# Kernel tuning notes

Hardware: AMD Instinct MI355X
Metric: run time of the kernel (lower is better)

Reference implementation:

```python
import jax, jax.numpy as jnp
import numpy as np

N_NODES = 50000
N_EDGES = 400000
N_GRAPHS = 256
D = 200
N_STEPS = 6


def setup_inputs() -> dict:
    key = jax.random.key(0)
    ks = jax.random.split(key, 10)
    s = 1.0 / np.sqrt(D)
    x = jax.random.normal(ks[0], (N_NODES, D), dtype=jnp.float32)
    edge_index = jax.random.randint(ks[1], (2, N_EDGES), 0, N_NODES, dtype=jnp.int64)
    batch = jnp.sort(jax.random.randint(ks[2], (N_NODES,), 0, N_GRAPHS, dtype=jnp.int64))
    ggnn_weight = jax.random.uniform(ks[3], (N_STEPS, D, D), jnp.float32, -s, s)
    w_ih = jax.random.uniform(ks[4], (3 * D, D), jnp.float32, -s, s)
    w_hh = jax.random.uniform(ks[5], (3 * D, D), jnp.float32, -s, s)
    b_ih = jax.random.uniform(ks[6], (3 * D,), jnp.float32, -s, s)
    b_hh = jax.random.uniform(ks[7], (3 * D,), jnp.float32, -s, s)
    cls_w = jax.random.uniform(ks[8], (2, D), jnp.float32, -s, s)
    cls_b = jax.random.uniform(ks[9], (2,), jnp.float32, -s, s)
    return {"x": x, "edge_index": edge_index, "batch": batch,
            "ggnn_weight": ggnn_weight, "w_ih": w_ih, "w_hh": w_hh,
            "b_ih": b_ih, "b_hh": b_hh, "cls_w": cls_w, "cls_b": cls_b}


def _gru_cell(m, h, w_ih, w_hh, b_ih, b_hh):
    gi = m @ w_ih.T + b_ih            # [N, 3D]
    gh = h @ w_hh.T + b_hh            # [N, 3D]
    i_r, i_z, i_n = jnp.split(gi, 3, axis=-1)
    h_r, h_z, h_n = jnp.split(gh, 3, axis=-1)
    r = jax.nn.sigmoid(i_r + h_r)
    z = jax.nn.sigmoid(i_z + h_z)
    n = jnp.tanh(i_n + r * h_n)
    return (1.0 - z) * n + z * h


def reference(x, edge_index, batch, ggnn_weight, w_ih, w_hh, b_ih, b_hh, cls_w, cls_b):
    src, dst = edge_index[0], edge_index[1]

    def step(h, W):
        m = h @ W                                        # [N, D]
        agg = jax.ops.segment_sum(m[src], dst, num_segments=N_NODES)  # scatter-add
        return _gru_cell(agg, h, w_ih, w_hh, b_ih, b_hh), None

    h, _ = jax.lax.scan(step, x, ggnn_weight)
    h = jax.nn.relu(h)
    pooled = jax.ops.segment_max(h, batch, num_segments=N_GRAPHS)    # [G, D]
    logits = pooled @ cls_w.T + cls_b                                # [G, 2]
    return jax.nn.sigmoid(logits)
```

## Files before the change

### kernel.cpp

```cpp
#include <hip/hip_runtime.h>
#include <cstdint>
#include <cstddef>

#define NN 50000
#define NE 400000
#define NG 256
#define DIM 200
#define NSTEPS 6

typedef unsigned int uint;
typedef unsigned short ushort;
typedef __attribute__((ext_vector_type(8))) short short8;
typedef __attribute__((ext_vector_type(4))) float f32x4;

#define GLL16(gsrc, ldst)                                                        \
  __builtin_amdgcn_global_load_lds(                                              \
      (const __attribute__((address_space(1))) void*)(gsrc),                     \
      (__attribute__((address_space(3))) void*)(ldst), 16, 0, 0)

__device__ __forceinline__ float bfu(ushort u) { return __uint_as_float((uint)u << 16); }
__device__ __forceinline__ uint packf(float v) {
  uint u = __float_as_uint(v);
  uint t = u + 0x7fffu + ((u >> 16) & 1u);
  uint hb = t & 0xffff0000u;
  float lo = v - __uint_as_float(hb);
  uint ul = __float_as_uint(lo);
  uint t2 = ul + 0x7fffu + ((ul >> 16) & 1u);
  return hb | (t2 >> 16);
}
__device__ __forceinline__ ushort bf16rn(float v) {
  uint u = __float_as_uint(v);
  return (ushort)((u + 0x7fffu + ((u >> 16) & 1u)) >> 16);
}
__device__ __forceinline__ float fsig(float x) {
  return __builtin_amdgcn_rcpf(1.f + __expf(-x));
}
__device__ __forceinline__ float ftanh(float x) {
  return 1.f - 2.f * __builtin_amdgcn_rcpf(__expf(2.f * x) + 1.f);
}

__global__ void k_zero_i32(int* __restrict__ p, int n) {
  for (int i = blockIdx.x * blockDim.x + threadIdx.x; i < n; i += gridDim.x * blockDim.x)
    p[i] = 0;
}
__global__ void k_zero_f32(float* __restrict__ p, int n) {
  for (int i = blockIdx.x * blockDim.x + threadIdx.x; i < n; i += gridDim.x * blockDim.x)
    p[i] = 0.f;
}
__global__ void k_hist(const int* __restrict__ dst, int* __restrict__ cnt, int nE) {
  int e = blockIdx.x * blockDim.x + threadIdx.x;
  if (e < nE) atomicAdd(&cnt[dst[e]], 1);
}

__global__ __launch_bounds__(256) void k_scan_blk(const int* __restrict__ cnt,
                                                  int* __restrict__ incl,
                                                  int* __restrict__ bsum, int n) {
  __shared__ int buf[256];
  int i = blockIdx.x * 256 + threadIdx.x;
  int v = (i < n) ? cnt[i] : 0;
  buf[threadIdx.x] = v;
  __syncthreads();
#pragma unroll
  for (int d = 1; d < 256; d <<= 1) {
    int t = (threadIdx.x >= d) ? buf[threadIdx.x - d] : 0;
    __syncthreads();
    buf[threadIdx.x] += t;
    __syncthreads();
  }
  if (i < n) incl[i] = buf[threadIdx.x];
  if (threadIdx.x == 255) bsum[blockIdx.x] = buf[255];
}
__global__ __launch_bounds__(256) void k_scan_top(int* __restrict__ bsum, int nb) {
  __shared__ int buf[256];
  int v = (threadIdx.x < nb) ? bsum[threadIdx.x] : 0;
  buf[threadIdx.x] = v;
  __syncthreads();
#pragma unroll
  for (int d = 1; d < 256; d <<= 1) {
    int t = (threadIdx.x >= d) ? buf[threadIdx.x - d] : 0;
    __syncthreads();
    buf[threadIdx.x] += t;
    __syncthreads();
  }
  if (threadIdx.x < nb) bsum[threadIdx.x] = buf[threadIdx.x] - v;
}
__global__ __launch_bounds__(256) void k_scan_fin(const int* __restrict__ cnt,
                                                  const int* __restrict__ incl,
                                                  const int* __restrict__ bsum,
                                                  int* __restrict__ off,
                                                  int* __restrict__ cursor, int n) {
  int i = blockIdx.x * 256 + threadIdx.x;
  if (i < n) {
    int o = incl[i] + bsum[blockIdx.x];
    off[i + 1] = o;
    cursor[i] = o - cnt[i];
  }
  if (i == 0) off[0] = 0;
}

__global__ void k_scatter(const int* __restrict__ dst, const int* __restrict__ src,
                          int* __restrict__ cursor, int* __restrict__ slist, int nE) {
  int e = blockIdx.x * blockDim.x + threadIdx.x;
  if (e < nE) {
    int d = dst[e];
    int pos = atomicAdd(&cursor[d], 1);
    slist[pos] = src[e];
  }
}

__global__ void k_pack_split(const float* __restrict__ x, ushort* __restrict__ hHi,
                             ushort* __restrict__ hLo, int n8) {
  for (int i = blockIdx.x * blockDim.x + threadIdx.x; i < n8;
       i += gridDim.x * blockDim.x) {
    const float* s = x + (size_t)i * 8;
    uint hi[4], lo[4];
#pragma unroll
    for (int j = 0; j < 4; ++j) {
      uint w0 = packf(s[j * 2]), w1 = packf(s[j * 2 + 1]);
      hi[j] = (w0 >> 16) | (w1 & 0xffff0000u);
      lo[j] = (w0 & 0xffffu) | (w1 << 16);
    }
    *reinterpret_cast<uint4*>(hHi + (size_t)i * 8) = make_uint4(hi[0], hi[1], hi[2], hi[3]);
    *reinterpret_cast<uint4*>(hLo + (size_t)i * 8) = make_uint4(lo[0], lo[1], lo[2], lo[3]);
  }
}

__global__ void k_pack_bf(const float* __restrict__ in, ushort* __restrict__ out, int n) {
  for (int i = blockIdx.x * blockDim.x + threadIdx.x; i < n; i += gridDim.x * blockDim.x)
    out[i] = bf16rn(in[i]);
}

#define GBM 64
#define GBN 64
#define GBK 8
__global__ __launch_bounds__(256) void k_gemm_wc(const float* __restrict__ gg,
                                                 const float* __restrict__ w_ih,
                                                 ushort* __restrict__ wcB) {
  __shared__ __align__(16) float As[GBK][GBM];
  __shared__ __align__(16) float Bs[GBK][GBN];
  int s = blockIdx.z;
  const float* A = gg + (size_t)s * DIM * DIM;
  ushort* out = wcB + (size_t)s * 3 * DIM * DIM;
  int tid = threadIdx.x;
  int row0 = blockIdx.y * GBM;
  int col0 = blockIdx.x * GBN;
  int ty = tid >> 4, tx = tid & 15;
  float acc[4][4] = {};
  for (int k0 = 0; k0 < DIM; k0 += GBK) {
    {
      int r = tid >> 2;
      int kk = (tid & 3) * 2;
      int gr = row0 + r;
      float2 v = make_float2(0.f, 0.f);
      if (gr < DIM) v = *reinterpret_cast<const float2*>(&A[(size_t)gr * DIM + k0 + kk]);
      As[kk][r] = v.x; As[kk + 1][r] = v.y;
    }
    {
      int n = tid >> 2;
      int kk = (tid & 3) * 2;
      int gn = col0 + n;
      float2 v = *reinterpret_cast<const float2*>(&w_ih[(size_t)gn * DIM + k0 + kk]);
      Bs[kk][n] = v.x; Bs[kk + 1][n] = v.y;
    }
    __syncthreads();
#pragma unroll
    for (int k = 0; k < GBK; ++k) {
      float4 av = *reinterpret_cast<const float4*>(&As[k][ty * 4]);
      float4 bv = *reinterpret_cast<const float4*>(&Bs[k][tx * 4]);
      float a[4] = {av.x, av.y, av.z, av.w};
      float b[4] = {bv.x, bv.y, bv.z, bv.w};
#pragma unroll
      for (int i = 0; i < 4; ++i)
#pragma unroll
        for (int j = 0; j < 4; ++j) acc[i][j] += a[i] * b[j];
    }
    __syncthreads();
  }
#pragma unroll
  for (int i = 0; i < 4; ++i) {
    int r = row0 + ty * 4 + i;
    if (r >= DIM) continue;
#pragma unroll
    for (int j = 0; j < 4; ++j) {
      int c = col0 + tx * 4 + j;
      out[(size_t)c * DIM + r] = bf16rn(acc[i][j]);
    }
  }
}

__global__ __launch_bounds__(256) void k_aggregate_hi(const ushort* __restrict__ hHi,
                                                      const int* __restrict__ off,
                                                      const int* __restrict__ slist,
                                                      ushort* __restrict__ aggHi) {
  int wid = blockIdx.x * 4 + (threadIdx.x >> 6);
  int half = (threadIdx.x >> 5) & 1;
  int node = wid * 2 + half;
  int lane32 = threadIdx.x & 31;
  bool nok = node < NN;
  bool act = (lane32 < 25) && nok;
  const uint4* hb = reinterpret_cast<const uint4*>(hHi);
  float a[8] = {};
  int beg = 0, end = 0;
  if (nok) { beg = off[node]; end = off[node + 1]; }
  int p = beg;
#define ACC8(q)                                                   \
  {                                                               \
    a[0] += __uint_as_float((q).x << 16);                         \
    a[1] += __uint_as_float((q).x & 0xffff0000u);                 \
    a[2] += __uint_as_float((q).y << 16);                         \
    a[3] += __uint_as_float((q).y & 0xffff0000u);                 \
    a[4] += __uint_as_float((q).z << 16);                         \
    a[5] += __uint_as_float((q).z & 0xffff0000u);                 \
    a[6] += __uint_as_float((q).w << 16);                         \
    a[7] += __uint_as_float((q).w & 0xffff0000u);                 \
  }
  for (; p + 3 < end; p += 4) {
    int s0 = slist[p], s1 = slist[p + 1], s2 = slist[p + 2], s3 = slist[p + 3];
    if (act) {
      uint4 q0 = hb[(size_t)s0 * 25 + lane32];
      uint4 q1 = hb[(size_t)s1 * 25 + lane32];
      uint4 q2 = hb[(size_t)s2 * 25 + lane32];
      uint4 q3 = hb[(size_t)s3 * 25 + lane32];
      ACC8(q0) ACC8(q1) ACC8(q2) ACC8(q3)
    }
  }
  for (; p < end; ++p) {
    int s = slist[p];
    if (act) {
      uint4 q = hb[(size_t)s * 25 + lane32];
      ACC8(q)
    }
  }
#undef ACC8
  if (act) {
    uint w[4];
#pragma unroll
    for (int j = 0; j < 4; ++j)
      w[j] = (uint)bf16rn(a[j * 2]) | ((uint)bf16rn(a[j * 2 + 1]) << 16);
    reinterpret_cast<uint4*>(aggHi)[(size_t)node * 25 + lane32] =
        make_uint4(w[0], w[1], w[2], w[3]);
  }
}

#define NPAN 391
#define PPC 6
#define NCHK 66
#define NCOLB 7
#define GRIDF 462

#define MFMA16(a, b, c) __builtin_amdgcn_mfma_f32_16x16x32_bf16(a, b, c, 0, 0, 0)

__global__ __launch_bounds__(256, 2) void k_fused_mfma(
    const ushort* __restrict__ aggHi, const ushort* __restrict__ hHi,
    const ushort* __restrict__ hLo,
    const ushort* __restrict__ wcB, const ushort* __restrict__ whB,
    const float* __restrict__ b_ih, const float* __restrict__ b_hh,
    ushort* __restrict__ hnHi, ushort* __restrict__ hnLo) {
  __shared__ uint4 Bb[6][25][32];

  int tid = threadIdx.x;
  int lane = tid & 63;
  int wv = tid >> 6;
  int lr = lane & 15;
  int kc = lane >> 4;

  int x = blockIdx.x & 7, ii = blockIdx.x >> 3;
  int work = (x < 6 ? x * 58 : 348 + (x - 6) * 57) + ii;
  int chunk = work / NCOLB;
  int col = work - chunk * NCOLB;
  int cc0 = col * 32;

  {
    uint4* BbF = &Bb[0][0][0];
    for (int i2 = 0; i2 < 19; ++i2) {
      int u = tid + i2 * 256;
      if (u < 4800) {
        int mat = u / 800;
        int rem = u - mat * 800;
        int ch = rem >> 5;
        int c = rem & 31;
        int gc = cc0 + c; if (gc > 199) gc = 199;
        const ushort* wsrc = (mat & 1) ? whB : wcB;
        GLL16(wsrc + (size_t)((mat >> 1) * DIM + gc) * DIM + ch * 8, BbF + u);
      }
    }
  }
  __syncthreads();

  for (int j = 0; j < PPC; ++j) {
    int p = chunk * PPC + j;
    if (p >= NPAN) break;
    int prow0 = p * 128;
    int r0 = prow0 + wv * 32 + lr;
    int r1 = r0 + 16;
    int rc0 = r0 < NN ? r0 : NN - 1;
    int rc1 = r1 < NN ? r1 : NN - 1;
    const ushort* a0 = aggHi + (size_t)rc0 * DIM;
    const ushort* a1 = aggHi + (size_t)rc1 * DIM;
    const ushort* h0 = hHi + (size_t)rc0 * DIM;
    const ushort* h1 = hHi + (size_t)rc1 * DIM;

    f32x4 acc[3][2][2][2] = {};
    short8 aq[3][2][2];

#define LDA(d, t)                                                              \
  {                                                                            \
    const bool v_ = ((t) < 6) || (kc == 0);                                    \
    const int of_ = v_ ? ((t) * 32 + kc * 8) : 0;                              \
    const short8 z_ = {0, 0, 0, 0, 0, 0, 0, 0};                                \
    aq[d][0][0] = v_ ? *reinterpret_cast<const short8*>(a0 + of_) : z_;        \
    aq[d][0][1] = v_ ? *reinterpret_cast<const short8*>(a1 + of_) : z_;        \
    aq[d][1][0] = v_ ? *reinterpret_cast<const short8*>(h0 + of_) : z_;        \
    aq[d][1][1] = v_ ? *reinterpret_cast<const short8*>(h1 + of_) : z_;        \
  }

    LDA(0, 0)
    LDA(1, 1)
#pragma unroll
    for (int t = 0; t < 7; ++t) {
      const int cur = t % 3;
      if (t < 5) LDA((t + 2) % 3, t + 2)
      int bch = t * 4 + kc; if (bch > 24) bch = 24;
#pragma unroll
      for (int g = 0; g < 3; ++g) {
#pragma unroll
        for (int ct = 0; ct < 2; ++ct) {
          short8 b1 = *reinterpret_cast<const short8*>(&Bb[g * 2 + 0][bch][ct * 16 + lr]);
          short8 b2 = *reinterpret_cast<const short8*>(&Bb[g * 2 + 1][bch][ct * 16 + lr]);
#pragma unroll
          for (int rf = 0; rf < 2; ++rf) {
            acc[g][0][rf][ct] = MFMA16(aq[cur][0][rf], b1, acc[g][0][rf][ct]);
            acc[g][1][rf][ct] = MFMA16(aq[cur][1][rf], b2, acc[g][1][rf][ct]);
          }
        }
      }
    }
#undef LDA

#pragma unroll
    for (int ct = 0; ct < 2; ++ct) {
      int c = cc0 + ct * 16 + lr;
      if (c >= DIM) continue;
      float bir = b_ih[c], biz = b_ih[DIM + c], bin = b_ih[2 * DIM + c];
      float bhr = b_hh[c], bhz = b_hh[DIM + c], bhn = b_hh[2 * DIM + c];
#pragma unroll
      for (int rf = 0; rf < 2; ++rf) {
#pragma unroll
        for (int qq = 0; qq < 4; ++qq) {
          int r_ = prow0 + wv * 32 + rf * 16 + kc * 4 + qq;
          if (r_ >= NN) continue;
          size_t base = (size_t)r_ * DIM + c;
          float gir = acc[0][0][rf][ct][qq] + bir;
          float giz = acc[1][0][rf][ct][qq] + biz;
          float gin = acc[2][0][rf][ct][qq] + bin;
          float ghr = acc[0][1][rf][ct][qq] + bhr;
          float ghz = acc[1][1][rf][ct][qq] + bhz;
          float ghn = acc[2][1][rf][ct][qq] + bhn;
          float rr = fsig(gir + ghr);
          float zz = fsig(giz + ghz);
          float nn = ftanh(gin + rr * ghn);
          float hv = bfu(hHi[base]) + bfu(hLo[base]);
          uint w = packf((1.f - zz) * nn + zz * hv);
          hnHi[base] = (ushort)(w >> 16);
          hnLo[base] = (ushort)(w & 0xffffu);
        }
      }
    }
  }
}

__global__ __launch_bounds__(256) void k_pool(const ushort* __restrict__ hHi,
                                              const ushort* __restrict__ hLo,
                                              const int* __restrict__ batch,
                                              float* __restrict__ pooled) {
  int i = blockIdx.x;
  int j = threadIdx.x;
  if (j < DIM) {
    int g = batch[i];
    size_t base = (size_t)i * DIM + j;
    float v = bfu(hHi[base]) + bfu(hLo[base]);
    v = v > 0.f ? v : 0.f;
    atomicMax((int*)&pooled[(size_t)g * DIM + j], __float_as_int(v));
  }
}

__global__ __launch_bounds__(256) void k_classify(const float* __restrict__ pooled,
                                                  const float* __restrict__ w,
                                                  const float* __restrict__ b,
                                                  float* __restrict__ out) {
  __shared__ float r0[256], r1[256];
  int g = blockIdx.x;
  int j = threadIdx.x;
  float p = (j < DIM) ? pooled[(size_t)g * DIM + j] : 0.f;
  r0[j] = (j < DIM) ? p * w[j] : 0.f;
  r1[j] = (j < DIM) ? p * w[DIM + j] : 0.f;
  __syncthreads();
  for (int d = 128; d > 0; d >>= 1) {
    if (j < d) { r0[j] += r0[j + d]; r1[j] += r1[j + d]; }
    __syncthreads();
  }
  if (j == 0) {
    out[g * 2 + 0] = 1.f / (1.f + expf(-(r0[0] + b[0])));
    out[g * 2 + 1] = 1.f / (1.f + expf(-(r1[0] + b[1])));
  }
}

extern "C" void kernel_launch(void* const* d_in, const int* in_sizes, int n_in,
                              void* d_out, int out_size, void* d_ws, size_t ws_size,
                              hipStream_t stream) {
  const float* x = (const float*)d_in[0];
  const int* edge_index = (const int*)d_in[1];
  const int* batch = (const int*)d_in[2];
  const float* ggnn_w = (const float*)d_in[3];
  const float* w_ih = (const float*)d_in[4];
  const float* w_hh = (const float*)d_in[5];
  const float* b_ih = (const float*)d_in[6];
  const float* b_hh = (const float*)d_in[7];
  const float* cls_w = (const float*)d_in[8];
  const float* cls_b = (const float*)d_in[9];
  float* out = (float*)d_out;

  const int* src = edge_index;
  const int* dst = edge_index + NE;

  char* wsb = (char*)d_ws;
  size_t off = 0;
  auto alloc = [&](size_t bytes) -> void* {
    void* p = wsb + off;
    off += (bytes + 255) & ~(size_t)255;
    return p;
  };
  ushort* hHiA = (ushort*)alloc((size_t)NN * DIM * 2);
  ushort* hLoA = (ushort*)alloc((size_t)NN * DIM * 2);
  ushort* hHiB = (ushort*)alloc((size_t)NN * DIM * 2);
  ushort* hLoB = (ushort*)alloc((size_t)NN * DIM * 2);
  ushort* aggHi = (ushort*)alloc((size_t)NN * DIM * 2);
  ushort* wcB = (ushort*)alloc((size_t)NSTEPS * 3 * DIM * DIM * 2);
  ushort* whB = (ushort*)alloc((size_t)3 * DIM * DIM * 2);
  float* pooled = (float*)alloc((size_t)NG * DIM * 4);
  int* indeg = (int*)alloc((size_t)NN * 4);
  int* offs = (int*)alloc((size_t)(NN + 1) * 4);
  int* incl = (int*)alloc((size_t)NN * 4);
  int* bsum = (int*)alloc((size_t)256 * 4);
  int* cursor = (int*)alloc((size_t)NN * 4);
  int* slist = (int*)alloc((size_t)NE * 4);
  if (off > ws_size) return;

  const int NB = (NN + 255) / 256;

  k_pack_split<<<2048, 256, 0, stream>>>(x, hHiA, hLoA, NN * DIM / 8);

  k_zero_i32<<<196, 256, 0, stream>>>(indeg, NN);
  k_hist<<<(NE + 255) / 256, 256, 0, stream>>>(dst, indeg, NE);
  k_scan_blk<<<NB, 256, 0, stream>>>(indeg, incl, bsum, NN);
  k_scan_top<<<1, 256, 0, stream>>>(bsum, NB);
  k_scan_fin<<<NB, 256, 0, stream>>>(indeg, incl, bsum, offs, cursor, NN);
  k_scatter<<<(NE + 255) / 256, 256, 0, stream>>>(dst, src, cursor, slist, NE);

  {
    dim3 g((3 * DIM + GBN - 1) / GBN, (DIM + GBM - 1) / GBM, NSTEPS);
    k_gemm_wc<<<g, 256, 0, stream>>>(ggnn_w, w_ih, wcB);
    k_pack_bf<<<512, 256, 0, stream>>>(w_hh, whB, 3 * DIM * DIM);
  }

  ushort* hHic = hHiA;
  ushort* hLoc = hLoA;
  ushort* hHin = hHiB;
  ushort* hLon = hLoB;
  for (int s = 0; s < NSTEPS; ++s) {
    k_aggregate_hi<<<(NN / 2 + 3) / 4, 256, 0, stream>>>(hHic, offs, slist, aggHi);
    k_fused_mfma<<<GRIDF, 256, 0, stream>>>(aggHi, hHic, hLoc,
                                            wcB + (size_t)s * 3 * DIM * DIM,
                                            whB, b_ih, b_hh, hHin, hLon);
    ushort* t;
    t = hHic; hHic = hHin; hHin = t;
    t = hLoc; hLoc = hLon; hLon = t;
  }

  k_zero_f32<<<200, 256, 0, stream>>>(pooled, NG * DIM);
  k_pool<<<NN, 256, 0, stream>>>(hHic, hLoc, batch, pooled);
  k_classify<<<NG, 256, 0, stream>>>(pooled, cls_w, cls_b, out);
}
```

Baseline: 700.0 us.

## Deepen A prefetch, preload epilogue h values, halve panels per block

The fused GRU MFMA kernel now gives each block 3 row panels instead of 6, which roughly doubles the grid, and the work mapping across the 8 XCD slices is rebalanced to match. The A-operand prefetch ring grows from 3 to 4 stages. The hHi/hLo values the epilogue needs are loaded into registers during the last MFMA iterations, so their latency overlaps compute instead of stalling the epilogue. The low-half bf16 pack now truncates instead of rounding, trimming epilogue ALU work at a tiny precision cost. In exchange, register pressure rises and each block reloads the weight tile into LDS over fewer panels.

```diff
diff --git a/kernel.cpp b/kernel.cpp
--- a/kernel.cpp
+++ b/kernel.cpp
@@ -27,6 +27,13 @@
   uint ul = __float_as_uint(lo);
   uint t2 = ul + 0x7fffu + ((ul >> 16) & 1u);
   return hb | (t2 >> 16);
+}
+__device__ __forceinline__ uint packf_tr(float v) {
+  uint u = __float_as_uint(v);
+  uint t = u + 0x7fffu + ((u >> 16) & 1u);
+  uint hb = t & 0xffff0000u;
+  float lo = v - __uint_as_float(hb);
+  return hb | (__float_as_uint(lo) >> 16);
 }
 __device__ __forceinline__ ushort bf16rn(float v) {
   uint u = __float_as_uint(v);
@@ -243,10 +250,10 @@
 }
 
 #define NPAN 391
-#define PPC 6
-#define NCHK 66
+#define PPC 3
+#define NCHK 131
 #define NCOLB 7
-#define GRIDF 462
+#define GRIDF 917
 
 #define MFMA16(a, b, c) __builtin_amdgcn_mfma_f32_16x16x32_bf16(a, b, c, 0, 0, 0)
 
@@ -265,7 +272,7 @@
   int kc = lane >> 4;
 
   int x = blockIdx.x & 7, ii = blockIdx.x >> 3;
-  int work = (x < 6 ? x * 58 : 348 + (x - 6) * 57) + ii;
+  int work = (x < 5 ? x * 115 : 575 + (x - 5) * 114) + ii;
   int chunk = work / NCOLB;
   int col = work - chunk * NCOLB;
   int cc0 = col * 32;
@@ -301,7 +308,8 @@
     const ushort* h1 = hHi + (size_t)rc1 * DIM;
 
     f32x4 acc[3][2][2][2] = {};
-    short8 aq[3][2][2];
+    short8 aq[4][2][2];
+    ushort hvh[2][2][4], hvl[2][2][4];
 
 #define LDA(d, t)                                                              \
   {                                                                            \
@@ -316,10 +324,28 @@
 
     LDA(0, 0)
     LDA(1, 1)
+    LDA(2, 2)
 #pragma unroll
     for (int t = 0; t < 7; ++t) {
-      const int cur = t % 3;
-      if (t < 5) LDA((t + 2) % 3, t + 2)
+      const int cur = t & 3;
+      if (t < 4) LDA((t + 3) & 3, t + 3)
+      if (t == 5) {
+#pragma unroll
+        for (int ct = 0; ct < 2; ++ct) {
+          int c = cc0 + ct * 16 + lr; if (c > 199) c = 199;
+#pragma unroll
+          for (int rf = 0; rf < 2; ++rf) {
+#pragma unroll
+            for (int qq = 0; qq < 4; ++qq) {
+              int r_ = prow0 + wv * 32 + rf * 16 + kc * 4 + qq;
+              int rc = r_ < NN ? r_ : NN - 1;
+              size_t base = (size_t)rc * DIM + c;
+              hvh[ct][rf][qq] = hHi[base];
+              hvl[ct][rf][qq] = hLo[base];
+            }
+          }
+        }
+      }
       int bch = t * 4 + kc; if (bch > 24) bch = 24;
 #pragma unroll
       for (int g = 0; g < 3; ++g) {
@@ -359,8 +385,8 @@
           float rr = fsig(gir + ghr);
           float zz = fsig(giz + ghz);
           float nn = ftanh(gin + rr * ghn);
-          float hv = bfu(hHi[base]) + bfu(hLo[base]);
-          uint w = packf((1.f - zz) * nn + zz * hv);
+          float hv = bfu(hvh[ct][rf][qq]) + bfu(hvl[ct][rf][qq]);
+          uint w = packf_tr((1.f - zz) * nn + zz * hv);
           hnHi[base] = (ushort)(w >> 16);
           hnLo[base] = (ushort)(w & 0xffffu);
         }
```

Result: faster. 669.9 us (-4.3%).
